# Kernel optimization log

Hardware: AMD Instinct MI355X
Metric: run time of the kernel (lower is better)

Reference implementation:

```python
import jax, jax.numpy as jnp
import numpy as np

F_DIM = 128; K_RBF = 64; NBLOCKS = 3; NUM_SCC = 1; IBEGIN = 4
N_RES_INT = 2; N_RES_AT = 2; N_RES_OUT = 1
NUM_OUTPUTS = 2001; NOUTS = NUM_OUTPUTS + 4  # +4 charge-equilibration channels when num_scc>0
N_ATOMS = 10000; DEG = 32; N_EDGES = N_ATOMS * DEG; NMOL = 64
CUTOFF = 10.0
LOG2 = 0.6931471805599453


def ssp(x):
    # shifted softplus
    return jax.nn.softplus(x) - LOG2


def _residual(x, W1, b1, W2, b2):
    y = ssp(x) @ W1 + b1
    return x + ssp(y) @ W2 + b2


def _forward(R, M, QaAlpha, QaBeta,
             em_W0, em_b0, em_W1, em_b1, em_W2, em_b2,
             iWrbf, iWi, ibi, iWj, ibj, irW1, irb1, irW2, irb2, iWout, ibout, iu,
             arW1, arb1, arW2, arb2, orW1, orb1, orW2, orb2, oW,
             Z, idx_i, idx_j, mol_idx):
    N = R.shape[0]
    dt = R.dtype
    # --- interatomic distances via neighbor gather ---
    Dvec = R[idx_i] - R[idx_j]                                # [E,3]
    Dij = jnp.sqrt(jax.nn.relu(jnp.sum(Dvec * Dvec, -1)))     # [E]
    # --- PhysNet-style exp-Gaussian RBF expansion with smooth cutoff ---
    mu = jnp.linspace(np.exp(-CUTOFF), 1.0, K_RBF).astype(dt)
    gamma = jnp.asarray((K_RBF / (2.0 * (1.0 - np.exp(-CUTOFF)))) ** 2, dt)
    t = Dij / CUTOFF
    cut = jnp.where(Dij < CUTOFF, 1.0 - 6.0 * t**5 + 15.0 * t**4 - 10.0 * t**3, 0.0)
    rbf = cut[:, None] * jnp.exp(-gamma * (jnp.exp(-Dij)[:, None] - mu) ** 2)  # [E,K]

    seg_mol = lambda v: jax.ops.segment_sum(v, mol_idx, num_segments=NMOL)
    Zf = Z.astype(dt)[:, None]
    QaA, QaB = QaAlpha, QaBeta
    QAlpha_mol = seg_mol(QaA)
    QBeta_mol = seg_mol(QaB)
    outputs = None
    nhloss = jnp.asarray(0.0, dt)
    for j in range(NUM_SCC + 1):
        # elemental-modes embedding: f = [Z, M, QaAlpha, QaBeta] -> F
        f = jnp.concatenate([Zf, M[:, None], QaA[:, None], QaB[:, None]], 1)  # [N,4]
        h = ssp(f @ em_W0 + em_b0)
        h = ssp(h @ em_W1 + em_b1)
        x = h @ em_W2 + em_b2                                 # [N,F]
        outputs = jnp.zeros((N, NOUTS), dt)
        nhloss = jnp.asarray(0.0, dt)
        lastout2 = None
        for i in range(NBLOCKS):
            # --- interaction (message passing: gather -> multiply -> segment_sum) ---
            xa = ssp(x)
            g = rbf @ iWrbf[i]                                # [E,F]
            xi = ssp(xa @ iWi[i] + ibi[i])                    # [N,F]
            xj = ssp(xa @ iWj[i] + ibj[i])                    # [N,F]
            m = xi + jax.ops.segment_sum(g * xj[idx_j], idx_i, num_segments=N)
            for r in range(N_RES_INT):
                m = _residual(m, irW1[i, r], irb1[i, r], irW2[i, r], irb2[i, r])
            m = ssp(m)
            x = iu[i] * x + m @ iWout[i] + ibout[i]           # gated update
            for r in range(N_RES_AT):
                x = _residual(x, arW1[i, r], arb1[i, r], arW2[i, r], arb2[i, r])
            # --- output block ---
            xo = x
            for r in range(N_RES_OUT):
                xo = _residual(xo, orW1[i, r], orb1[i, r], orW2[i, r], orb2[i, r])
            out = ssp(xo) @ oW[i]                             # [N,NOUTS]
            outputs = outputs + out
            if j == NUM_SCC:
                out2 = out[IBEGIN:] ** 2                      # row slice, as in source
                if i > 0:
                    nhloss = nhloss + jnp.mean(out2 / (out2 + lastout2 + 1e-7))
                lastout2 = out2
        # --- NSE charge equilibration (per-molecule segment sums) ---
        QaA_n, faA = outputs[:, 0], outputs[:, 1]
        QaB_n, faB = outputs[:, 2], outputs[:, 3]
        QaA = QaA_n + faA * ((QAlpha_mol - seg_mol(QaA_n)) / seg_mol(faA))[mol_idx]
        QaB = QaB_n + faB * ((QBeta_mol - seg_mol(QaB_n)) / seg_mol(faB))[mol_idx]
    outputs = outputs[:, IBEGIN:]
    outputs = jnp.concatenate([outputs[:, :1], jax.nn.relu(outputs[:, 1:])], 1)
    return outputs, Dij, nhloss


def setup_inputs() -> dict:
    key = jax.random.key(0)
    ks = iter(jax.random.split(key, 64))
    nrm = lambda shp, scale: jax.random.normal(next(ks), shp, jnp.float32) * scale
    F, K, B = F_DIM, K_RBF, NBLOCKS
    s = F ** -0.5
    inp = {}
    inp["R"] = jax.random.uniform(next(ks), (N_ATOMS, 3), jnp.float32, 0.0, 12.0)
    inp["M"] = jax.random.uniform(next(ks), (N_ATOMS,), jnp.float32, 1.0, 32.0)
    inp["QaAlpha"] = nrm((N_ATOMS,), 0.1)
    inp["QaBeta"] = nrm((N_ATOMS,), 0.1)
    # elemental-modes MLP 4 -> F -> F -> F
    inp["em_W0"] = nrm((4, F), 0.5); inp["em_b0"] = nrm((F,), 0.01)
    inp["em_W1"] = nrm((F, F), s);   inp["em_b1"] = nrm((F,), 0.01)
    inp["em_W2"] = nrm((F, F), s);   inp["em_b2"] = nrm((F,), 0.01)
    # interaction blocks (stacked over NBLOCKS)
    inp["iWrbf"] = nrm((B, K, F), K ** -0.5)
    inp["iWi"] = nrm((B, F, F), s); inp["ibi"] = nrm((B, F), 0.01)
    inp["iWj"] = nrm((B, F, F), s); inp["ibj"] = nrm((B, F), 0.01)
    inp["irW1"] = nrm((B, N_RES_INT, F, F), s); inp["irb1"] = nrm((B, N_RES_INT, F), 0.01)
    inp["irW2"] = nrm((B, N_RES_INT, F, F), s); inp["irb2"] = nrm((B, N_RES_INT, F), 0.01)
    inp["iWout"] = nrm((B, F, F), s); inp["ibout"] = nrm((B, F), 0.01)
    inp["iu"] = jnp.ones((B, F), jnp.float32)
    inp["arW1"] = nrm((B, N_RES_AT, F, F), s); inp["arb1"] = nrm((B, N_RES_AT, F), 0.01)
    inp["arW2"] = nrm((B, N_RES_AT, F, F), s); inp["arb2"] = nrm((B, N_RES_AT, F), 0.01)
    inp["orW1"] = nrm((B, N_RES_OUT, F, F), s); inp["orb1"] = nrm((B, N_RES_OUT, F), 0.01)
    inp["orW2"] = nrm((B, N_RES_OUT, F, F), s); inp["orb2"] = nrm((B, N_RES_OUT, F), 0.01)
    inp["oW"] = nrm((B, F, NOUTS), s)
    # integer graph structure
    inp["Z"] = jax.random.randint(next(ks), (N_ATOMS,), 1, 36, jnp.int32)
    idx_i = jnp.repeat(jnp.arange(N_ATOMS, dtype=jnp.int32), DEG)
    rnd = jax.random.randint(next(ks), (N_EDGES,), 1, N_ATOMS, jnp.int32)
    inp["idx_i"] = idx_i
    inp["idx_j"] = (idx_i + rnd) % N_ATOMS  # never self -> Dij > 0
    inp["mol_idx"] = ((jnp.arange(N_ATOMS) * NMOL) // N_ATOMS).astype(jnp.int32)
    return inp


def reference(R, M, QaAlpha, QaBeta,
              em_W0, em_b0, em_W1, em_b1, em_W2, em_b2,
              iWrbf, iWi, ibi, iWj, ibj, irW1, irb1, irW2, irb2, iWout, ibout, iu,
              arW1, arb1, arW2, arb2, orW1, orb1, orW2, orb2, oW,
              Z, idx_i, idx_j, mol_idx):
    return _forward(R, M, QaAlpha, QaBeta,
                    em_W0, em_b0, em_W1, em_b1, em_W2, em_b2,
                    iWrbf, iWi, ibi, iWj, ibj, irW1, irb1, irW2, irb2, iWout, ibout, iu,
                    arW1, arb1, arW2, arb2, orW1, orb1, orW2, orb2, oW,
                    Z, idx_i, idx_j, mol_idx)
```

## Files before the change

### kernel.cpp

```cpp
#include <hip/hip_runtime.h>
#include <math.h>

#define NA 10000
#define NAP 10048
#define FD 128
#define KR 64
#define DEGC 32
#define NE (NA*DEGC)
#define NOUTS_C 2005
#define NOUT_FINAL 2001

typedef __attribute__((ext_vector_type(8))) short bh8;
typedef __attribute__((ext_vector_type(4))) float fx4;

__device__ __forceinline__ float sspf(float x){
    float ex = __expf(-fabsf(x));
    return fmaxf(x, 0.0f) + __logf(1.0f + ex) - 0.6931471805599453f;
}
__device__ __forceinline__ unsigned short f2bf(float x){
    unsigned int u = __float_as_uint(x);
    unsigned int r = (u + 0x7fffu + ((u >> 16) & 1u)) >> 16;
    return (unsigned short)r;
}
__device__ __forceinline__ float bf2f(unsigned short u){
    return __uint_as_float(((unsigned int)u) << 16);
}
__device__ __forceinline__ fx4 mfma16(bh8 a, bh8 b, fx4 c){
    return __builtin_amdgcn_mfma_f32_16x16x32_bf16(a, b, c, 0, 0, 0);
}
__device__ __forceinline__ void gll16(const void* g, void* l){
    __builtin_amdgcn_global_load_lds(
        (const __attribute__((address_space(1))) unsigned int*)g,
        (__attribute__((address_space(3))) unsigned int*)l, 16, 0, 0);
}

__global__ void k_dij(const float* __restrict__ R, const int* __restrict__ idx_i,
                      const int* __restrict__ idx_j, float* __restrict__ dij_out){
    int e = blockIdx.x*256 + threadIdx.x;
    if (e >= NE) return;
    int i = idx_i[e], j = idx_j[e];
    float dx = R[i*3+0] - R[j*3+0];
    float dy = R[i*3+1] - R[j*3+1];
    float dz = R[i*3+2] - R[j*3+2];
    dij_out[e] = sqrtf(fmaxf(dx*dx + dy*dy + dz*dz, 0.0f));
}

__global__ void k_init(const float* __restrict__ QaAin, const float* __restrict__ QaBin,
                       const int* __restrict__ mol, float* __restrict__ QaA,
                       float* __restrict__ QaB, float* __restrict__ QAmol,
                       float* __restrict__ QBmol){
    int a = blockIdx.x*256 + threadIdx.x;
    if (a >= NA) return;
    float qa = QaAin[a], qb = QaBin[a];
    QaA[a] = qa; QaB[a] = qb;
    int m = mol[a];
    atomicAdd(&QAmol[m], qa);
    atomicAdd(&QBmol[m], qb);
}

__global__ void k_cvtW(const float* __restrict__ em_W1, const float* __restrict__ em_W2,
                       const float* __restrict__ iWi, const float* __restrict__ iWj,
                       const float* __restrict__ iWout, const float* __restrict__ irW1,
                       const float* __restrict__ irW2, const float* __restrict__ arW1,
                       const float* __restrict__ arW2, const float* __restrict__ orW1,
                       const float* __restrict__ orW2, short* __restrict__ img){
    int gid = blockIdx.x*256 + threadIdx.x;
    if (gid >= 41*2048) return;
    int m = gid >> 11;
    int f = gid & 2047;
    int l15 = f & 15, t = f >> 4;
    int g = t & 3, u = t >> 2;
    int kk = u & 3, cg = u >> 2;
    const float* src; int mm;
    if      (m < 1){ src = em_W1; mm = m; }
    else if (m < 2){ src = em_W2; mm = m-1; }
    else if (m < 5){ src = iWi;   mm = m-2; }
    else if (m < 8){ src = iWj;   mm = m-5; }
    else if (m < 11){ src = iWout; mm = m-8; }
    else if (m < 17){ src = irW1;  mm = m-11; }
    else if (m < 23){ src = irW2;  mm = m-17; }
    else if (m < 29){ src = arW1;  mm = m-23; }
    else if (m < 35){ src = arW2;  mm = m-29; }
    else if (m < 38){ src = orW1;  mm = m-35; }
    else            { src = orW2;  mm = m-38; }
    src += (size_t)mm * 16384;
    int n = cg*16 + l15;
    int k0 = (kk*4 + g)*8;
    bh8 pk;
    #pragma unroll
    for (int j = 0; j < 8; ++j) pk[j] = (short)f2bf(src[(k0+j)*128 + n]);
    *(bh8*)&img[m*16384 + f*8] = pk;
}

__global__ void k_cvtB(const float* __restrict__ em_b1, const float* __restrict__ em_b2,
                       const float* __restrict__ ibi, const float* __restrict__ ibj,
                       const float* __restrict__ ibout, const float* __restrict__ irb1,
                       const float* __restrict__ irb2, const float* __restrict__ arb1,
                       const float* __restrict__ arb2, const float* __restrict__ orb1,
                       const float* __restrict__ orb2, const float* __restrict__ iu,
                       float* __restrict__ bimg){
    int gid = blockIdx.x*256 + threadIdx.x;
    if (gid >= 44*128) return;
    int m = gid >> 7, c = gid & 127;
    float v;
    if      (m < 1)  v = em_b1[c];
    else if (m < 2)  v = em_b2[c];
    else if (m < 5)  v = ibi[(m-2)*128+c];
    else if (m < 8)  v = ibj[(m-5)*128+c];
    else if (m < 11) v = ibout[(m-8)*128+c];
    else if (m < 17) v = irb1[(m-11)*128+c];
    else if (m < 23) v = irb2[(m-17)*128+c];
    else if (m < 29) v = arb1[(m-23)*128+c];
    else if (m < 35) v = arb2[(m-29)*128+c];
    else if (m < 38) v = orb1[(m-35)*128+c];
    else if (m < 41) v = orb2[(m-38)*128+c];
    else             v = iu[(m-41)*128+c];
    bimg[gid] = v;
}

__global__ void k_cvt_wrbf(const float* __restrict__ iWrbf, short* __restrict__ img){
    int gid = blockIdx.x*256 + threadIdx.x;
    if (gid >= 3*1024) return;
    int i = gid >> 10;
    int loc = gid & 1023;
    int n = loc >> 3, s = loc & 7;
    const float* src = iWrbf + (size_t)i*8192;
    int kbase = (s ^ (n&7)) * 8;
    bh8 pk;
    #pragma unroll
    for (int j = 0; j < 8; ++j) pk[j] = (short)f2bf(src[(kbase+j)*128 + n]);
    *(bh8*)&img[i*8192 + n*64 + s*8] = pk;
}

__global__ void k_cvt_oW(const float* __restrict__ oW, short* __restrict__ img){
    int gid = blockIdx.x*256 + threadIdx.x;
    if (gid >= 98304) return;
    int l15 = gid & 15;
    int g = (gid >> 4) & 3;
    int nt = (gid >> 6) & 7;
    int rest = gid >> 9;
    int kk2 = rest % 12, cg = rest / 12;
    int seg = kk2 >> 2;
    int n = cg*128 + nt*16 + l15;
    int kbase = (kk2 & 3)*32 + g*8;
    bh8 pk;
    #pragma unroll
    for (int j = 0; j < 8; ++j){
        float v = (n < NOUTS_C) ? oW[((size_t)seg*128 + kbase + j)*NOUTS_C + n] : 0.0f;
        pk[j] = (short)f2bf(v);
    }
    *(bh8*)&img[(size_t)gid*8] = pk;
}

__device__ __forceinline__ void loadB8(const short* __restrict__ W, int g, int l15, int wv, bh8 b[8]){
    const bh8* Wf = (const bh8*)W;
    const int cgA = wv*2, cgB = wv*2 + 1;
    #pragma unroll
    for (int kk = 0; kk < 4; ++kk){
        b[kk]   = Wf[((cgA*4+kk)*4+g)*16 + l15];
        b[4+kk] = Wf[((cgB*4+kk)*4+g)*16 + l15];
    }
}
__device__ __forceinline__ void gemmB(const short* As, const bh8 b[8], int g, int l15, fx4 acc[2]){
    #pragma unroll
    for (int kk = 0; kk < 4; ++kk){
        int q = kk*4 + g;
        bh8 a = *(const bh8*)&As[l15*128 + ((q ^ (l15&7))*8)];
        acc[0] = mfma16(a, b[kk],   acc[0]);
        acc[1] = mfma16(a, b[4+kk], acc[1]);
    }
}
#define ZACC2 { acc[0]=(fx4){0,0,0,0}; acc[1]=(fx4){0,0,0,0}; }

__device__ __forceinline__ void epiS_ts(short* dst, fx4 acc[2], const float* b,
                                        int g, int c0, int c1){
    float b0 = b[c0], b1 = b[c1];
    #pragma unroll
    for (int r = 0; r < 4; ++r){
        int row = g*4 + r;
        dst[row*128 + (((c0>>3) ^ (row&7))*8) + (c0&7)] = (short)f2bf(sspf(acc[0][r] + b0));
        dst[row*128 + (((c1>>3) ^ (row&7))*8) + (c1&7)] = (short)f2bf(sspf(acc[1][r] + b1));
    }
}
__device__ __forceinline__ void epiS_xadd(float xr[2][4], fx4 acc[2], const float* b,
                                          int c0, int c1){
    float b0 = b[c0], b1 = b[c1];
    #pragma unroll
    for (int r = 0; r < 4; ++r){
        xr[0][r] += acc[0][r] + b0;
        xr[1][r] += acc[1][r] + b1;
    }
}
__device__ __forceinline__ void writeS_xr(short* dst, float xr[2][4], int g, int c0, int c1){
    #pragma unroll
    for (int r = 0; r < 4; ++r){
        int row = g*4 + r;
        dst[row*128 + (((c0>>3) ^ (row&7))*8) + (c0&7)] = (short)f2bf(sspf(xr[0][r]));
        dst[row*128 + (((c1>>3) ^ (row&7))*8) + (c1&7)] = (short)f2bf(sspf(xr[1][r]));
    }
}
__device__ __forceinline__ void storeS_xr(float* dst, float xr[2][4], int r0, int g, int c0, int c1){
    #pragma unroll
    for (int r = 0; r < 4; ++r){
        int row = r0 + g*4 + r;
        dst[(size_t)row*FD + c0] = xr[0][r];
        dst[(size_t)row*FD + c1] = xr[1][r];
    }
}
__device__ __forceinline__ void storeS_ssp(float* dst, fx4 acc[2], const float* b,
                                           int r0, int g, int c0, int c1){
    float b0 = b[c0], b1 = b[c1];
    #pragma unroll
    for (int r = 0; r < 4; ++r){
        int row = r0 + g*4 + r;
        dst[(size_t)row*FD + c0] = sspf(acc[0][r] + b0);
        dst[(size_t)row*FD + c1] = sspf(acc[1][r] + b1);
    }
}
__device__ __forceinline__ void stage_A16(short* As, const float* src, int r0, int tid){
    int row = tid >> 4, cb = tid & 15;
    const float* p = src + (size_t)(r0+row)*FD + cb*8;
    float4 u = *(const float4*)p, v = *(const float4*)(p+4);
    float vv[8] = {u.x,u.y,u.z,u.w,v.x,v.y,v.z,v.w};
    bh8 pk;
    #pragma unroll
    for (int t = 0; t < 8; ++t) pk[t] = (short)f2bf(sspf(vv[t]));
    *(bh8*)&As[row*128 + ((cb ^ (row&7))*8)] = pk;
}

__global__ __launch_bounds__(256) void k_pre(
    const short* __restrict__ wimg, const float* __restrict__ bimg,
    const int* __restrict__ Z, const float* __restrict__ M,
    const float* __restrict__ QaA, const float* __restrict__ QaB,
    const float* __restrict__ em_W0, const float* __restrict__ em_b0,
    float* __restrict__ x, float* __restrict__ xi, float* __restrict__ xj)
{
    __shared__ __align__(16) short As[2048];
    __shared__ __align__(16) short Ts[2048];
    __shared__ float fs[16][4];
    const int tid = threadIdx.x, wv = tid>>6, ln = tid&63, g = ln>>4, l15 = ln&15;
    const int r0 = blockIdx.x*16;
    const int c0 = wv*32 + l15, c1 = c0 + 16;
    bh8 bU[8], bV[8];
    if (tid < 64){
        int rr = tid>>2, k = tid&3;
        int a = r0 + rr;
        fs[rr][k] = (k==0) ? (float)Z[a] : (k==1) ? M[a] : (k==2) ? QaA[a] : QaB[a];
    }
    __syncthreads();
    {
        int row = tid>>4, cb = tid&15;
        bh8 pk;
        #pragma unroll
        for (int t = 0; t < 8; ++t){
            int c = cb*8 + t;
            float v = sspf(em_b0[c] + fs[row][0]*em_W0[c] + fs[row][1]*em_W0[128+c]
                           + fs[row][2]*em_W0[256+c] + fs[row][3]*em_W0[384+c]);
            pk[t] = (short)f2bf(v);
        }
        *(bh8*)&As[row*128 + ((cb ^ (row&7))*8)] = pk;
    }
    loadB8(wimg + 0*16384, g, l15, wv, bU);
    __syncthreads();
    fx4 acc[2];
    float xr[2][4];
    ZACC2; gemmB(As, bU, g, l15, acc);
    loadB8(wimg + 1*16384, g, l15, wv, bV);
    epiS_ts(Ts, acc, bimg + 0*128, g, c0, c1);
    __syncthreads();
    ZACC2; gemmB(Ts, bV, g, l15, acc);
    loadB8(wimg + 2*16384, g, l15, wv, bU);
    {
        const float* b = bimg + 1*128;
        float b0 = b[c0], b1 = b[c1];
        #pragma unroll
        for (int r = 0; r < 4; ++r){
            xr[0][r] = acc[0][r] + b0;
            xr[1][r] = acc[1][r] + b1;
        }
    }
    storeS_xr(x, xr, r0, g, c0, c1);
    writeS_xr(As, xr, g, c0, c1);
    __syncthreads();
    ZACC2; gemmB(As, bU, g, l15, acc);
    loadB8(wimg + 5*16384, g, l15, wv, bV);
    storeS_ssp(xi, acc, bimg + 2*128, r0, g, c0, c1);
    ZACC2; gemmB(As, bV, g, l15, acc);
    storeS_ssp(xj, acc, bimg + 5*128, r0, g, c0, c1);
}

__global__ __launch_bounds__(256) void k_post(
    const short* __restrict__ wimg, const float* __restrict__ bimg,
    const float* __restrict__ mb, float* __restrict__ x,
    short* __restrict__ Aimg, float* __restrict__ xi, float* __restrict__ xj,
    int i, int dodual)
{
    __shared__ __align__(16) short As[2048];
    __shared__ __align__(16) short Ts[2048];
    const int tid = threadIdx.x, wv = tid>>6, ln = tid&63, g = ln>>4, l15 = ln&15;
    const int r0 = blockIdx.x*16;
    const int c0 = wv*32 + l15, c1 = c0 + 16;
    bh8 bU[8], bV[8];
    float xr[2][4];
    #pragma unroll
    for (int r = 0; r < 4; ++r){
        size_t row = (size_t)(r0 + g*4 + r);
        xr[0][r] = mb[row*FD + c0];
        xr[1][r] = mb[row*FD + c1];
    }
    stage_A16(As, mb, r0, tid);
    loadB8(wimg + (size_t)(11+2*i)*16384, g, l15, wv, bU);
    __syncthreads();
    fx4 acc[2];
    ZACC2; gemmB(As, bU, g, l15, acc);
    loadB8(wimg + (size_t)(17+2*i)*16384, g, l15, wv, bV);
    epiS_ts(Ts, acc, bimg + (11+2*i)*128, g, c0, c1);
    __syncthreads();
    ZACC2; gemmB(Ts, bV, g, l15, acc);
    loadB8(wimg + (size_t)(12+2*i)*16384, g, l15, wv, bU);
    epiS_xadd(xr, acc, bimg + (17+2*i)*128, c0, c1);
    writeS_xr(As, xr, g, c0, c1);
    __syncthreads();
    ZACC2; gemmB(As, bU, g, l15, acc);
    loadB8(wimg + (size_t)(18+2*i)*16384, g, l15, wv, bV);
    epiS_ts(Ts, acc, bimg + (12+2*i)*128, g, c0, c1);
    __syncthreads();
    ZACC2; gemmB(Ts, bV, g, l15, acc);
    loadB8(wimg + (size_t)(8+i)*16384, g, l15, wv, bU);
    epiS_xadd(xr, acc, bimg + (18+2*i)*128, c0, c1);
    writeS_xr(As, xr, g, c0, c1);
    __syncthreads();
    ZACC2; gemmB(As, bU, g, l15, acc);
    loadB8(wimg + (size_t)(23+2*i)*16384, g, l15, wv, bV);
    {
        const float* bb = bimg + (8+i)*128;
        const float* uu = bimg + (41+i)*128;
        float b0 = bb[c0], b1 = bb[c1], u0 = uu[c0], u1 = uu[c1];
        #pragma unroll
        for (int r = 0; r < 4; ++r){
            size_t row = (size_t)(r0 + g*4 + r);
            xr[0][r] = u0*x[row*FD + c0] + acc[0][r] + b0;
            xr[1][r] = u1*x[row*FD + c1] + acc[1][r] + b1;
        }
    }
    writeS_xr(Ts, xr, g, c0, c1);
    __syncthreads();
    ZACC2; gemmB(Ts, bV, g, l15, acc);
    loadB8(wimg + (size_t)(29+2*i)*16384, g, l15, wv, bU);
    epiS_ts(As, acc, bimg + (23+2*i)*128, g, c0, c1);
    __syncthreads();
    ZACC2; gemmB(As, bU, g, l15, acc);
    loadB8(wimg + (size_t)(24+2*i)*16384, g, l15, wv, bV);
    epiS_xadd(xr, acc, bimg + (29+2*i)*128, c0, c1);
    writeS_xr(Ts, xr, g, c0, c1);
    __syncthreads();
    ZACC2; gemmB(Ts, bV, g, l15, acc);
    loadB8(wimg + (size_t)(30+2*i)*16384, g, l15, wv, bU);
    epiS_ts(As, acc, bimg + (24+2*i)*128, g, c0, c1);
    __syncthreads();
    ZACC2; gemmB(As, bU, g, l15, acc);
    loadB8(wimg + (size_t)(dodual ? (3+i) : (35+i))*16384, g, l15, wv, bV);
    epiS_xadd(xr, acc, bimg + (30+2*i)*128, c0, c1);
    storeS_xr(x, xr, r0, g, c0, c1);
    writeS_xr(Ts, xr, g, c0, c1);
    __syncthreads();
    if (dodual){
        ZACC2; gemmB(Ts, bV, g, l15, acc);
        loadB8(wimg + (size_t)(6+i)*16384, g, l15, wv, bU);
        storeS_ssp(xi, acc, bimg + (3+i)*128, r0, g, c0, c1);
        ZACC2; gemmB(Ts, bU, g, l15, acc);
        loadB8(wimg + (size_t)(35+i)*16384, g, l15, wv, bV);
        storeS_ssp(xj, acc, bimg + (6+i)*128, r0, g, c0, c1);
        ZACC2; gemmB(Ts, bV, g, l15, acc);
        loadB8(wimg + (size_t)(38+i)*16384, g, l15, wv, bU);
        epiS_ts(As, acc, bimg + (35+i)*128, g, c0, c1);
    } else {
        ZACC2; gemmB(Ts, bV, g, l15, acc);
        loadB8(wimg + (size_t)(38+i)*16384, g, l15, wv, bU);
        epiS_ts(As, acc, bimg + (35+i)*128, g, c0, c1);
    }
    __syncthreads();
    ZACC2; gemmB(As, bU, g, l15, acc);
    {
        const float* bb = bimg + (38+i)*128;
        float b0 = bb[c0], b1 = bb[c1];
        #pragma unroll
        for (int r = 0; r < 4; ++r){
            int row = r0 + g*4 + r;
            float v0 = xr[0][r] + acc[0][r] + b0;
            float v1 = xr[1][r] + acc[1][r] + b1;
            int k0 = i*128 + c0, k1 = i*128 + c1;
            Aimg[(size_t)row*384 + (((k0>>3) ^ (row&7))*8) + (k0&7)] = (short)f2bf(sspf(v0));
            Aimg[(size_t)row*384 + (((k1>>3) ^ (row&7))*8) + (k1&7)] = (short)f2bf(sspf(v1));
        }
    }
}

__global__ __launch_bounds__(256) void k_agg_mfma(
    const float* __restrict__ dij, const short* __restrict__ wri,
    const int* __restrict__ idxj, const float* __restrict__ xi,
    const float* __restrict__ xj, float* __restrict__ mout,
    float gamma, float mu0, float dmu)
{
    __shared__ short Rb[256*64];
    __shared__ short Wr[128*64];
    __shared__ int Jd[256];
    const int tid = threadIdx.x;
    const int wv = tid >> 6, ln = tid & 63;
    const int e0 = blockIdx.x * 256;
    {
        const char* g2 = (const char*)wri;
        char* l2 = (char*)Wr;
        #pragma unroll
        for (int i = 0; i < 4; ++i){
            int off = wv*4096 + i*1024;
            gll16(g2 + off + ln*16, l2 + off);
        }
        Jd[tid] = idxj[e0 + tid];
    }
    {
        float d = dij[e0 + tid];
        float t = d * 0.1f;
        float cut = 0.0f;
        if (d < 10.0f){
            float t2 = t*t, t3 = t2*t, t4 = t2*t2, t5 = t4*t;
            cut = 1.0f - 6.0f*t5 + 15.0f*t4 - 10.0f*t3;
        }
        float ed = __expf(-d);
        int row = tid;
        #pragma unroll
        for (int s = 0; s < 8; ++s){
            bh8 pk;
            #pragma unroll
            for (int jj = 0; jj < 8; ++jj){
                float u = ed - (mu0 + (float)(s*8+jj)*dmu);
                pk[jj] = (short)f2bf(cut * __expf(-gamma*u*u));
            }
            *(bh8*)&Rb[row*64 + ((s ^ (row&7))*8)] = pk;
        }
    }
    __syncthreads();
    const int g = ln >> 4, l15 = ln & 15;
    bh8 a[4][2];
    #pragma unroll
    for (int mt = 0; mt < 4; ++mt){
        int el = wv*64 + mt*16 + l15;
        #pragma unroll
        for (int kk = 0; kk < 2; ++kk)
            a[mt][kk] = *(const bh8*)&Rb[el*64 + (((kk*4+g) ^ (el&7))*8)];
    }
    float pa[2][8];
    #pragma unroll
    for (int q = 0; q < 8; ++q){ pa[0][q]=0.f; pa[1][q]=0.f; }
    #pragma unroll
    for (int h = 0; h < 2; ++h){
        fx4 acc[4][4];
        #pragma unroll
        for (int mt = 0; mt < 4; ++mt)
            #pragma unroll
            for (int nt = 0; nt < 4; ++nt) acc[mt][nt] = (fx4){0,0,0,0};
        #pragma unroll
        for (int kk = 0; kk < 2; ++kk){
            #pragma unroll
            for (int nt = 0; nt < 4; ++nt){
                int n = h*64 + nt*16 + l15;
                bh8 b = *(const bh8*)&Wr[n*64 + (((kk*4+g) ^ (n&7))*8)];
                #pragma unroll
                for (int mt = 0; mt < 4; ++mt)
                    acc[mt][nt] = mfma16(a[mt][kk], b, acc[mt][nt]);
            }
        }
        #pragma unroll
        for (int mt = 0; mt < 4; ++mt){
            int at = mt >> 1;
            int jv[4];
            #pragma unroll
            for (int r = 0; r < 4; ++r) jv[r] = Jd[wv*64 + mt*16 + g*4 + r];
            #pragma unroll
            for (int nt = 0; nt < 4; ++nt){
                int col = h*64 + nt*16 + l15;
                float s = 0.f;
                #pragma unroll
                for (int r = 0; r < 4; ++r)
                    s += acc[mt][nt][r] * xj[(size_t)jv[r]*FD + col];
                pa[at][h*4+nt] += s;
            }
        }
    }
    #pragma unroll
    for (int at = 0; at < 2; ++at)
        #pragma unroll
        for (int q = 0; q < 8; ++q){
            float v = pa[at][q];
            v += __shfl_xor(v, 16);
            v += __shfl_xor(v, 32);
            pa[at][q] = v;
        }
    if (g == 0){
        #pragma unroll
        for (int at = 0; at < 2; ++at){
            int ga = blockIdx.x*8 + wv*2 + at;
            #pragma unroll
            for (int q = 0; q < 8; ++q){
                int col = (q>>2)*64 + (q&3)*16 + l15;
                mout[(size_t)ga*FD + col] = xi[(size_t)ga*FD + col] + pa[at][q];
            }
        }
    }
}

__global__ void k_out4all(const short* __restrict__ Aimg, const float* __restrict__ oW,
                          float* __restrict__ out4){
    int gid = blockIdx.x*256 + threadIdx.x;
    int a = gid >> 6;
    int lane = threadIdx.x & 63;
    if (a >= NA) return;
    float p0=0.f, p1=0.f, p2=0.f, p3=0.f;
    #pragma unroll
    for (int seg = 0; seg < 3; ++seg){
        const float* oWs = oW + (size_t)seg*FD*NOUTS_C;
        int k0 = seg*128 + lane, k1 = k0 + 64;
        float y0 = bf2f((unsigned short)Aimg[(size_t)a*384 + (((k0>>3) ^ (a&7))*8) + (k0&7)]);
        float y1 = bf2f((unsigned short)Aimg[(size_t)a*384 + (((k1>>3) ^ (a&7))*8) + (k1&7)]);
        const float* w0 = oWs + (size_t)lane*NOUTS_C;
        const float* w1 = oWs + (size_t)(lane+64)*NOUTS_C;
        p0 += y0*w0[0] + y1*w1[0];
        p1 += y0*w0[1] + y1*w1[1];
        p2 += y0*w0[2] + y1*w1[2];
        p3 += y0*w0[3] + y1*w1[3];
    }
    #pragma unroll
    for (int off = 32; off > 0; off >>= 1){
        p0 += __shfl_down(p0, off);
        p1 += __shfl_down(p1, off);
        p2 += __shfl_down(p2, off);
        p3 += __shfl_down(p3, off);
    }
    if (lane == 0){
        out4[a*4+0] = p0; out4[a*4+1] = p1;
        out4[a*4+2] = p2; out4[a*4+3] = p3;
    }
}

__global__ void k_molsum(const float* __restrict__ out4, const int* __restrict__ mol,
                         float* __restrict__ sums){
    int a = blockIdx.x*256 + threadIdx.x;
    if (a >= NA) return;
    int m = mol[a];
    atomicAdd(&sums[m],     out4[a*4+0]);
    atomicAdd(&sums[64+m],  out4[a*4+1]);
    atomicAdd(&sums[128+m], out4[a*4+2]);
    atomicAdd(&sums[192+m], out4[a*4+3]);
}

__global__ void k_qaupd(const float* __restrict__ out4, const int* __restrict__ mol,
                        const float* __restrict__ sums, const float* __restrict__ QAmol,
                        const float* __restrict__ QBmol, float* __restrict__ QaA,
                        float* __restrict__ QaB){
    int a = blockIdx.x*256 + threadIdx.x;
    if (a >= NA) return;
    int m = mol[a];
    float qa_n = out4[a*4+0], fa = out4[a*4+1];
    float qb_n = out4[a*4+2], fb = out4[a*4+3];
    QaA[a] = qa_n + fa * ((QAmol[m] - sums[m])     / sums[64+m]);
    QaB[a] = qb_n + fb * ((QBmol[m] - sums[128+m]) / sums[192+m]);
}

__global__ __launch_bounds__(256, 1) void k_final8(
    const short* __restrict__ Aimg, const short* __restrict__ oWfrag,
    float* __restrict__ outp, float* __restrict__ nh_acc)
{
    const int tid = threadIdx.x, wv = tid>>6, ln = tid&63, g = ln>>4, l15 = ln&15;
    const int r0 = blockIdx.x*64 + wv*16;
    const int arow = r0 + l15;
    bh8 af[12];
    #pragma unroll
    for (int kk2 = 0; kk2 < 12; ++kk2){
        int s = kk2*4 + g;
        af[kk2] = *(const bh8*)&Aimg[(size_t)arow*384 + ((s ^ (l15&7))*8)];
    }
    float nh = 0.f;
    const int cg0 = blockIdx.y*4;
    const bh8* Bf = (const bh8*)oWfrag + (size_t)cg0*6144;
    bh8 bU[8], bV[8];
    #pragma unroll
    for (int nt = 0; nt < 8; ++nt) bU[nt] = Bf[(nt*4 + g)*16 + l15];
    #pragma unroll
    for (int cgl = 0; cgl < 4; ++cgl){
        const int cg = cg0 + cgl;
        const bh8* Bc = (const bh8*)oWfrag + (size_t)cg*6144;
        const bh8* Bn = Bc + 6144;
        fx4 osum[8], p2[8];
        #pragma unroll
        for (int nt = 0; nt < 8; ++nt){ osum[nt]=(fx4){0,0,0,0}; p2[nt]=(fx4){0,0,0,0}; }
        #pragma unroll
        for (int seg = 0; seg < 3; ++seg){
            fx4 acc[8];
            #pragma unroll
            for (int nt = 0; nt < 8; ++nt) acc[nt] = (fx4){0,0,0,0};
            #pragma unroll
            for (int kkl = 0; kkl < 4; ++kkl){
                const int kk2 = seg*4 + kkl;
                if ((kk2 & 1) == 0){
                    #pragma unroll
                    for (int nt = 0; nt < 8; ++nt)
                        bV[nt] = Bc[(((kk2+1)*8 + nt)*4 + g)*16 + l15];
                    #pragma unroll
                    for (int nt = 0; nt < 8; ++nt)
                        acc[nt] = mfma16(af[kk2], bU[nt], acc[nt]);
                } else {
                    if (kk2 < 11){
                        #pragma unroll
                        for (int nt = 0; nt < 8; ++nt)
                            bU[nt] = Bc[(((kk2+1)*8 + nt)*4 + g)*16 + l15];
                    } else if (cgl < 3){
                        #pragma unroll
                        for (int nt = 0; nt < 8; ++nt)
                            bU[nt] = Bn[(nt*4 + g)*16 + l15];
                    }
                    #pragma unroll
                    for (int nt = 0; nt < 8; ++nt)
                        acc[nt] = mfma16(af[kk2], bV[nt], acc[nt]);
                }
            }
            #pragma unroll
            for (int nt = 0; nt < 8; ++nt)
            #pragma unroll
            for (int r = 0; r < 4; ++r){
                float o = acc[nt][r];
                osum[nt][r] += o;
                if (seg > 0){
                    int A = r0 + g*4 + r;
                    int col = cg*128 + nt*16 + l15;
                    if (A >= 4 && A < NA && col < NOUTS_C){
                        float o2 = o*o;
                        float den = o2 + p2[nt][r] + 1e-7f;
                        float rr;
                        asm("v_rcp_f32 %0, %1" : "=v"(rr) : "v"(den));
                        nh += o2 * rr;
                    }
                }
                p2[nt][r] = o*o;
            }
        }
        #pragma unroll
        for (int nt = 0; nt < 8; ++nt){
            int col = cg*128 + nt*16 + l15;
            #pragma unroll
            for (int r = 0; r < 4; ++r){
                int A = r0 + g*4 + r;
                if (A < NA && col >= 4 && col < NOUTS_C){
                    float v = osum[nt][r];
                    if (col > 4) v = fmaxf(v, 0.f);
                    outp[(size_t)A*NOUT_FINAL + (col - 4)] = v;
                }
            }
        }
    }
    #pragma unroll
    for (int off = 32; off > 0; off >>= 1) nh += __shfl_down(nh, off);
    if (ln == 0) atomicAdd(nh_acc, nh);
}

__global__ void k_finalize(const float* __restrict__ nh_acc, float* __restrict__ nh_out){
    *nh_out = *nh_acc * (1.0f / (float)((NA - 4) * NOUTS_C));
}

extern "C" void kernel_launch(void* const* d_in, const int* in_sizes, int n_in,
                              void* d_out, int out_size, void* d_ws, size_t ws_size,
                              hipStream_t stream)
{
    const float* R       = (const float*)d_in[0];
    const float* M       = (const float*)d_in[1];
    const float* QaAlpha = (const float*)d_in[2];
    const float* QaBeta  = (const float*)d_in[3];
    const float* em_W0   = (const float*)d_in[4];
    const float* em_b0   = (const float*)d_in[5];
    const float* em_W1   = (const float*)d_in[6];
    const float* em_b1   = (const float*)d_in[7];
    const float* em_W2   = (const float*)d_in[8];
    const float* em_b2   = (const float*)d_in[9];
    const float* iWrbf   = (const float*)d_in[10];
    const float* iWi     = (const float*)d_in[11];
    const float* ibi     = (const float*)d_in[12];
    const float* iWj     = (const float*)d_in[13];
    const float* ibj     = (const float*)d_in[14];
    const float* irW1    = (const float*)d_in[15];
    const float* irb1    = (const float*)d_in[16];
    const float* irW2    = (const float*)d_in[17];
    const float* irb2    = (const float*)d_in[18];
    const float* iWout   = (const float*)d_in[19];
    const float* ibout   = (const float*)d_in[20];
    const float* iu      = (const float*)d_in[21];
    const float* arW1    = (const float*)d_in[22];
    const float* arb1    = (const float*)d_in[23];
    const float* arW2    = (const float*)d_in[24];
    const float* arb2    = (const float*)d_in[25];
    const float* orW1    = (const float*)d_in[26];
    const float* orb1    = (const float*)d_in[27];
    const float* orW2    = (const float*)d_in[28];
    const float* orb2    = (const float*)d_in[29];
    const float* oW      = (const float*)d_in[30];
    const int*   Z       = (const int*)d_in[31];
    const int*   idx_i   = (const int*)d_in[32];
    const int*   idx_j   = (const int*)d_in[33];
    const int*   mol     = (const int*)d_in[34];

    float* out    = (float*)d_out;
    float* dij    = out + (size_t)NA*NOUT_FINAL;
    float* nh_out = dij + NE;

    float* fbase = (float*)d_ws;
    size_t fo = 0;
    float* x    = fbase + fo; fo += (size_t)NA*FD;
    float* xi   = fbase + fo; fo += (size_t)NA*FD;
    float* xj   = fbase + fo; fo += (size_t)NA*FD;
    float* mb   = fbase + fo; fo += (size_t)NA*FD;
    float* out4 = fbase + fo; fo += (size_t)NA*4;
    float* sums = fbase + fo; fo += 256;
    float* QAmol= fbase + fo; fo += 64;
    float* QBmol= fbase + fo; fo += 64;
    float* nhac = fbase + fo; fo += 1;
    float* QaA  = fbase + fo; fo += NA;
    float* QaB  = fbase + fo; fo += NA;
    float* bimg = fbase + fo; fo += 44*128;
    size_t sboff = ((fo*4 + 63) / 64) * 64;
    short* sbase = (short*)((char*)d_ws + sboff);
    size_t so = 0;
    short* wimg   = sbase + so; so += (size_t)41*16384;
    short* wrbf   = sbase + so; so += (size_t)3*8192;
    short* oWfrag = sbase + so; so += (size_t)98304*8;
    short* Aimg   = sbase + so; so += (size_t)NAP*384;

    hipMemsetAsync(sums, 0, (size_t)(256 + 64 + 64 + 1)*sizeof(float), stream);
    hipMemsetAsync(Aimg + (size_t)NA*384, 0, (size_t)(NAP-NA)*384*sizeof(short), stream);

    k_cvtW<<<(41*2048+255)/256, 256, 0, stream>>>(em_W1, em_W2, iWi, iWj, iWout,
                                                  irW1, irW2, arW1, arW2, orW1, orW2, wimg);
    k_cvtB<<<(44*128+255)/256, 256, 0, stream>>>(em_b1, em_b2, ibi, ibj, ibout,
                                                 irb1, irb2, arb1, arb2, orb1, orb2, iu, bimg);
    k_cvt_wrbf<<<(3*1024+255)/256, 256, 0, stream>>>(iWrbf, wrbf);
    k_cvt_oW<<<(98304+255)/256, 256, 0, stream>>>(oW, oWfrag);

    k_dij<<<(NE+255)/256, 256, 0, stream>>>(R, idx_i, idx_j, dij);
    k_init<<<(NA+255)/256, 256, 0, stream>>>(QaAlpha, QaBeta, mol, QaA, QaB, QAmol, QBmol);

    double expn = exp(-10.0);
    float gamma = (float)pow(64.0/(2.0*(1.0-expn)), 2.0);
    float mu0 = (float)expn;
    float dmu = (float)((1.0-expn)/63.0);

    for (int j = 0; j <= 1; ++j){
        k_pre<<<625, 256, 0, stream>>>(wimg, bimg, Z, M, QaA, QaB, em_W0, em_b0, x, xi, xj);
        for (int i = 0; i < 3; ++i){
            k_agg_mfma<<<1250, 256, 0, stream>>>(dij, wrbf + (size_t)i*8192, idx_j, xi, xj, mb,
                                                 gamma, mu0, dmu);
            k_post<<<625, 256, 0, stream>>>(wimg, bimg, mb, x, Aimg, xi, xj, i, (i<2) ? 1 : 0);
        }
        if (j == 0){
            k_out4all<<<(NA*64)/256, 256, 0, stream>>>(Aimg, oW, out4);
            k_molsum<<<(NA+255)/256, 256, 0, stream>>>(out4, mol, sums);
            k_qaupd<<<(NA+255)/256, 256, 0, stream>>>(out4, mol, sums, QAmol, QBmol, QaA, QaB);
        }
    }
    k_final8<<<dim3(157,4), 256, 0, stream>>>(Aimg, oWfrag, out, nhac);
    k_finalize<<<1, 1, 0, stream>>>(nhac, nh_out);
}
```

Before: 972.6 us.

## Build RBF fragments in registers and give each final-GEMM wave two row tiles

```diff
diff --git a/kernel.cpp b/kernel.cpp
--- a/kernel.cpp
+++ b/kernel.cpp
@@ -396,13 +396,12 @@
     }
 }
 
-__global__ __launch_bounds__(256) void k_agg_mfma(
+__global__ __launch_bounds__(256) void k_agg2(
     const float* __restrict__ dij, const short* __restrict__ wri,
     const int* __restrict__ idxj, const float* __restrict__ xi,
     const float* __restrict__ xj, float* __restrict__ mout,
     float gamma, float mu0, float dmu)
 {
-    __shared__ short Rb[256*64];
     __shared__ short Wr[128*64];
     __shared__ int Jd[256];
     const int tid = threadIdx.x;
@@ -418,8 +417,12 @@
         }
         Jd[tid] = idxj[e0 + tid];
     }
-    {
-        float d = dij[e0 + tid];
+    const int g = ln >> 4, l15 = ln & 15;
+    bh8 a[4][2];
+    #pragma unroll
+    for (int mt = 0; mt < 4; ++mt){
+        int el = wv*64 + mt*16 + l15;
+        float d = dij[e0 + el];
         float t = d * 0.1f;
         float cut = 0.0f;
         if (d < 10.0f){
@@ -427,28 +430,19 @@
             cut = 1.0f - 6.0f*t5 + 15.0f*t4 - 10.0f*t3;
         }
         float ed = __expf(-d);
-        int row = tid;
-        #pragma unroll
-        for (int s = 0; s < 8; ++s){
+        #pragma unroll
+        for (int kk = 0; kk < 2; ++kk){
             bh8 pk;
             #pragma unroll
-            for (int jj = 0; jj < 8; ++jj){
-                float u = ed - (mu0 + (float)(s*8+jj)*dmu);
-                pk[jj] = (short)f2bf(cut * __expf(-gamma*u*u));
+            for (int j = 0; j < 8; ++j){
+                int k = (kk*4 + g)*8 + j;
+                float u = ed - (mu0 + (float)k*dmu);
+                pk[j] = (short)f2bf(cut * __expf(-gamma*u*u));
             }
-            *(bh8*)&Rb[row*64 + ((s ^ (row&7))*8)] = pk;
-        }
-    }
-    __syncthreads();
-    const int g = ln >> 4, l15 = ln & 15;
-    bh8 a[4][2];
-    #pragma unroll
-    for (int mt = 0; mt < 4; ++mt){
-        int el = wv*64 + mt*16 + l15;
-        #pragma unroll
-        for (int kk = 0; kk < 2; ++kk)
-            a[mt][kk] = *(const bh8*)&Rb[el*64 + (((kk*4+g) ^ (el&7))*8)];
-    }
+            a[mt][kk] = pk;
+        }
+    }
+    __syncthreads();
     float pa[2][8];
     #pragma unroll
     for (int q = 0; q < 8; ++q){ pa[0][q]=0.f; pa[1][q]=0.f; }
@@ -566,18 +560,18 @@
     QaB[a] = qb_n + fb * ((QBmol[m] - sums[128+m]) / sums[192+m]);
 }
 
-__global__ __launch_bounds__(256, 1) void k_final8(
+__global__ __launch_bounds__(128, 1) void k_final9(
     const short* __restrict__ Aimg, const short* __restrict__ oWfrag,
     float* __restrict__ outp, float* __restrict__ nh_acc)
 {
     const int tid = threadIdx.x, wv = tid>>6, ln = tid&63, g = ln>>4, l15 = ln&15;
-    const int r0 = blockIdx.x*64 + wv*16;
-    const int arow = r0 + l15;
-    bh8 af[12];
+    const int r0 = blockIdx.x*64 + wv*32;
+    bh8 af0[12], af1[12];
     #pragma unroll
     for (int kk2 = 0; kk2 < 12; ++kk2){
         int s = kk2*4 + g;
-        af[kk2] = *(const bh8*)&Aimg[(size_t)arow*384 + ((s ^ (l15&7))*8)];
+        af0[kk2] = *(const bh8*)&Aimg[(size_t)(r0+l15)*384    + ((s ^ (l15&7))*8)];
+        af1[kk2] = *(const bh8*)&Aimg[(size_t)(r0+16+l15)*384 + ((s ^ (l15&7))*8)];
     }
     float nh = 0.f;
     const int cg0 = blockIdx.y*4;
@@ -590,14 +584,17 @@
         const int cg = cg0 + cgl;
         const bh8* Bc = (const bh8*)oWfrag + (size_t)cg*6144;
         const bh8* Bn = Bc + 6144;
-        fx4 osum[8], p2[8];
-        #pragma unroll
-        for (int nt = 0; nt < 8; ++nt){ osum[nt]=(fx4){0,0,0,0}; p2[nt]=(fx4){0,0,0,0}; }
+        fx4 osum0[8], p20[8], osum1[8], p21[8];
+        #pragma unroll
+        for (int nt = 0; nt < 8; ++nt){
+            osum0[nt]=(fx4){0,0,0,0}; p20[nt]=(fx4){0,0,0,0};
+            osum1[nt]=(fx4){0,0,0,0}; p21[nt]=(fx4){0,0,0,0};
+        }
         #pragma unroll
         for (int seg = 0; seg < 3; ++seg){
-            fx4 acc[8];
-            #pragma unroll
-            for (int nt = 0; nt < 8; ++nt) acc[nt] = (fx4){0,0,0,0};
+            fx4 acc0[8], acc1[8];
+            #pragma unroll
+            for (int nt = 0; nt < 8; ++nt){ acc0[nt]=(fx4){0,0,0,0}; acc1[nt]=(fx4){0,0,0,0}; }
             #pragma unroll
             for (int kkl = 0; kkl < 4; ++kkl){
                 const int kk2 = seg*4 + kkl;
@@ -606,8 +603,10 @@
                     for (int nt = 0; nt < 8; ++nt)
                         bV[nt] = Bc[(((kk2+1)*8 + nt)*4 + g)*16 + l15];
                     #pragma unroll
-                    for (int nt = 0; nt < 8; ++nt)
-                        acc[nt] = mfma16(af[kk2], bU[nt], acc[nt]);
+                    for (int nt = 0; nt < 8; ++nt){
+                        acc0[nt] = mfma16(af0[kk2], bU[nt], acc0[nt]);
+                        acc1[nt] = mfma16(af1[kk2], bU[nt], acc1[nt]);
+                    }
                 } else {
                     if (kk2 < 11){
                         #pragma unroll
@@ -619,40 +618,62 @@
                             bU[nt] = Bn[(nt*4 + g)*16 + l15];
                     }
                     #pragma unroll
-                    for (int nt = 0; nt < 8; ++nt)
-                        acc[nt] = mfma16(af[kk2], bV[nt], acc[nt]);
+                    for (int nt = 0; nt < 8; ++nt){
+                        acc0[nt] = mfma16(af0[kk2], bV[nt], acc0[nt]);
+                        acc1[nt] = mfma16(af1[kk2], bV[nt], acc1[nt]);
+                    }
                 }
             }
             #pragma unroll
             for (int nt = 0; nt < 8; ++nt)
             #pragma unroll
             for (int r = 0; r < 4; ++r){
-                float o = acc[nt][r];
-                osum[nt][r] += o;
+                float o0 = acc0[nt][r], o1 = acc1[nt][r];
+                osum0[nt][r] += o0;
+                osum1[nt][r] += o1;
                 if (seg > 0){
-                    int A = r0 + g*4 + r;
                     int col = cg*128 + nt*16 + l15;
-                    if (A >= 4 && A < NA && col < NOUTS_C){
-                        float o2 = o*o;
-                        float den = o2 + p2[nt][r] + 1e-7f;
-                        float rr;
-                        asm("v_rcp_f32 %0, %1" : "=v"(rr) : "v"(den));
-                        nh += o2 * rr;
+                    if (col < NOUTS_C){
+                        int A0 = r0 + g*4 + r;
+                        if (A0 >= 4 && A0 < NA){
+                            float o2 = o0*o0;
+                            float den = o2 + p20[nt][r] + 1e-7f;
+                            float rr;
+                            asm("v_rcp_f32 %0, %1" : "=v"(rr) : "v"(den));
+                            nh += o2 * rr;
+                        }
+                        int A1 = r0 + 16 + g*4 + r;
+                        if (A1 >= 4 && A1 < NA){
+                            float o2 = o1*o1;
+                            float den = o2 + p21[nt][r] + 1e-7f;
+                            float rr;
+                            asm("v_rcp_f32 %0, %1" : "=v"(rr) : "v"(den));
+                            nh += o2 * rr;
+                        }
                     }
                 }
-                p2[nt][r] = o*o;
+                p20[nt][r] = o0*o0;
+                p21[nt][r] = o1*o1;
             }
         }
         #pragma unroll
         for (int nt = 0; nt < 8; ++nt){
             int col = cg*128 + nt*16 + l15;
-            #pragma unroll
-            for (int r = 0; r < 4; ++r){
-                int A = r0 + g*4 + r;
-                if (A < NA && col >= 4 && col < NOUTS_C){
-                    float v = osum[nt][r];
-                    if (col > 4) v = fmaxf(v, 0.f);
-                    outp[(size_t)A*NOUT_FINAL + (col - 4)] = v;
+            if (col >= 4 && col < NOUTS_C){
+                #pragma unroll
+                for (int r = 0; r < 4; ++r){
+                    int A0 = r0 + g*4 + r;
+                    if (A0 < NA){
+                        float v = osum0[nt][r];
+                        if (col > 4) v = fmaxf(v, 0.f);
+                        outp[(size_t)A0*NOUT_FINAL + (col - 4)] = v;
+                    }
+                    int A1 = r0 + 16 + g*4 + r;
+                    if (A1 < NA){
+                        float v = osum1[nt][r];
+                        if (col > 4) v = fmaxf(v, 0.f);
+                        outp[(size_t)A1*NOUT_FINAL + (col - 4)] = v;
+                    }
                 }
             }
         }
@@ -753,8 +774,8 @@
     for (int j = 0; j <= 1; ++j){
         k_pre<<<625, 256, 0, stream>>>(wimg, bimg, Z, M, QaA, QaB, em_W0, em_b0, x, xi, xj);
         for (int i = 0; i < 3; ++i){
-            k_agg_mfma<<<1250, 256, 0, stream>>>(dij, wrbf + (size_t)i*8192, idx_j, xi, xj, mb,
-                                                 gamma, mu0, dmu);
+            k_agg2<<<1250, 256, 0, stream>>>(dij, wrbf + (size_t)i*8192, idx_j, xi, xj, mb,
+                                             gamma, mu0, dmu);
             k_post<<<625, 256, 0, stream>>>(wimg, bimg, mb, x, Aimg, xi, xj, i, (i<2) ? 1 : 0);
         }
         if (j == 0){
@@ -763,6 +784,6 @@
             k_qaupd<<<(NA+255)/256, 256, 0, stream>>>(out4, mol, sums, QAmol, QBmol, QaA, QaB);
         }
     }
-    k_final8<<<dim3(157,4), 256, 0, stream>>>(Aimg, oWfrag, out, nhac);
+    k_final9<<<dim3(157,4), 128, 0, stream>>>(Aimg, oWfrag, out, nhac);
     k_finalize<<<1, 1, 0, stream>>>(nhac, nh_out);
 }
```

Result: slower. 1.163 ms (+19.5%).
